# Kernel tuning notes

Measured on AMD Instinct MI355X. Metric: run time of the kernel, lower is better.

The kernel has to match this reference:

```python
import jax, jax.numpy as jnp
import numpy as np

B, S, D, E, H, K = 4, 4096, 256, 8, 512, 2  # batch, seq, d_model, n_experts, ffn_hidden(=2*D), top_k


def setup_inputs() -> dict:
    key = jax.random.key(0)
    ks = jax.random.split(key, 6)
    x = jax.random.normal(ks[0], (B, S, D), jnp.float32)
    Wg = jax.random.normal(ks[1], (D, E), jnp.float32) * 0.02
    bg = jnp.zeros((E,), jnp.float32)
    W1 = jax.random.normal(ks[2], (E, D, H), jnp.float32) * 0.02
    b1 = jnp.zeros((E, H), jnp.float32)
    W2 = jax.random.normal(ks[3], (E, H, D), jnp.float32) * 0.02
    b2 = jnp.zeros((E, D), jnp.float32)
    return {"x": x, "Wg": Wg, "bg": bg, "W1": W1, "b1": b1, "W2": W2, "b2": b2}


def reference(x, Wg, bg, W1, b1, W2, b2):
    Bv, Sv, Dv = x.shape
    # Gate: linear -> top_k indices. NOTE: the original computes softmax(top_k scores)
    # but never uses the probabilities in the combine, so only indices matter.
    gate_scores = x @ Wg + bg                      # [B,S,E]
    _, idx = jax.lax.top_k(gate_scores, K)          # [B,S,K] (distinct experts per token)
    # Boolean membership mask per expert (0/1), matching (expert_indices == i).any(-1)
    mask = jax.nn.one_hot(idx, E, dtype=x.dtype).sum(axis=-2)  # [B,S,E]

    xf = x.reshape(-1, Dv)                          # [T,D]
    mf = mask.reshape(-1, E)                        # [T,E]
    # Dense all-experts FFN, masked combine (faithful to unweighted scatter-add).
    h = jax.nn.gelu(jnp.einsum('td,edh->teh', xf, W1) + b1[None], approximate=False)  # [T,E,H]
    y = jnp.einsum('teh,ehd->ted', h, W2) + b2[None]                                   # [T,E,D]
    out = jnp.einsum('ted,te->td', y, mf)                                              # [T,D]
    return out.reshape(Bv, Sv, Dv)
```

## Files before the change

### kernel.cpp

```cpp
#include <hip/hip_runtime.h>
#include <hip/hip_bf16.h>

#define T_TOK 16384
#define DM 256
#define NE 8
#define HF 512
#define TM 64
#define XS_LD 264
#define HC_LD 264

typedef __bf16 bf16x8 __attribute__((ext_vector_type(8)));
typedef float f32x4 __attribute__((ext_vector_type(4)));
typedef unsigned short u16x8 __attribute__((ext_vector_type(8)));

__device__ __forceinline__ unsigned short f2bf(float f) {
  unsigned u = __float_as_uint(f);
  u += 0x7fffu + ((u >> 16) & 1u);
  return (unsigned short)(u >> 16);
}

__device__ __forceinline__ float gelu_f(float v) {
  float s = fabsf(v) * 0.70710678118654752f;
  float t = __builtin_amdgcn_rcpf(1.0f + 0.3275911f * s);
  float p = t * (0.254829592f +
            t * (-0.284496736f +
            t * (1.421413741f +
            t * (-1.453152027f + t * 1.061405429f))));
  float e = 1.0f - p * __expf(-s * s);
  e = copysignf(e, v);
  return 0.5f * v * (1.0f + e);
}

__global__ __launch_bounds__(256) void gate_kernel(
    const float* __restrict__ x, const float* __restrict__ Wg,
    const float* __restrict__ bg, int* __restrict__ cnts, int* __restrict__ list) {
  __shared__ float wg_s[DM * NE];
  __shared__ int hist[NE], base_s[NE], rank[NE];
  int tid = threadIdx.x;
#pragma unroll
  for (int i = 0; i < NE; i++) wg_s[tid * NE + i] = Wg[tid * NE + i];
  if (tid < NE) { hist[tid] = 0; rank[tid] = 0; }
  __syncthreads();

  int tl = tid >> 2;
  int cg = tid & 3;
  int t = blockIdx.x * 64 + tl;
  const float* xr = x + (size_t)t * DM + cg * 64;
  double acc[NE];
#pragma unroll
  for (int i = 0; i < NE; i++) acc[i] = 0.0;
  for (int d = 0; d < 64; d += 4) {
    float4 xv = *reinterpret_cast<const float4*>(xr + d);
    const float* w0 = &wg_s[(cg * 64 + d) * NE];
#pragma unroll
    for (int i = 0; i < NE; i++) {
      acc[i] += (double)xv.x * (double)w0[i] + (double)xv.y * (double)w0[NE + i] +
                (double)xv.z * (double)w0[2 * NE + i] + (double)xv.w * (double)w0[3 * NE + i];
    }
  }
#pragma unroll
  for (int i = 0; i < NE; i++) {
    acc[i] += __shfl_xor(acc[i], 1, 64);
    acc[i] += __shfl_xor(acc[i], 2, 64);
    acc[i] += (double)bg[i];
  }
  int e1 = 0;
#pragma unroll
  for (int i = 1; i < NE; i++) if (acc[i] > acc[e1]) e1 = i;
  int e2 = -1;
#pragma unroll
  for (int i = 0; i < NE; i++) {
    if (i == e1) continue;
    if (e2 < 0 || acc[i] > acc[e2]) e2 = i;
  }

  if (cg == 0) {
    atomicAdd(&hist[e1], 1);
    atomicAdd(&hist[e2], 1);
  }
  __syncthreads();
  if (tid < NE) base_s[tid] = atomicAdd(&cnts[tid], hist[tid]);
  __syncthreads();
  if (cg == 0) {
    int r1 = atomicAdd(&rank[e1], 1);
    list[e1 * T_TOK + base_s[e1] + r1] = t;
    int r2 = atomicAdd(&rank[e2], 1);
    list[e2 * T_TOK + base_s[e2] + r2] = t;
  }
}

__global__ __launch_bounds__(256) void pack_kernel(
    const float* __restrict__ in, unsigned short* __restrict__ out, int K, int N) {
  int idx = blockIdx.x * 256 + threadIdx.x;
  int n = idx & (N - 1);
  int rest = idx / N;
  int kq = rest & ((K >> 3) - 1);
  int eidx = rest / (K >> 3);
  int k0 = kq * 8;
  const float* src = in + ((size_t)eidx * K + k0) * N + n;
  u16x8 pk;
#pragma unroll
  for (int j = 0; j < 8; j++) pk[j] = f2bf(src[(size_t)j * N]);
  size_t baseo = (size_t)eidx * K * N +
                 (size_t)((n >> 4) * (K >> 5) + (k0 >> 5)) * 512 +
                 (size_t)(((k0 >> 3) & 3) * 128 + (n & 15) * 8);
  *reinterpret_cast<u16x8*>(out + baseo) = pk;
}

__global__ __launch_bounds__(512, 4) void ffn_kernel(
    const float* __restrict__ x, const unsigned short* __restrict__ w1p,
    const float* __restrict__ b1, const unsigned short* __restrict__ w2p,
    const float* __restrict__ b2, const int* __restrict__ cnts,
    const int* __restrict__ list, float* __restrict__ out) {
  __shared__ unsigned short Xs[TM * XS_LD];
  __shared__ unsigned short Hc[TM * HC_LD];
  __shared__ int tok[TM];

  int e = blockIdx.x >> 8;
  int tile = blockIdx.x & 255;
  int cnt = cnts[e];
  int base = tile * TM;
  if (base >= cnt) return;
  int rowsv = min(TM, cnt - base);

  int tid = threadIdx.x;
  {
    int r = tid >> 3, cg = tid & 7;
    int token = -1;
    if (r < rowsv) token = list[e * T_TOK + base + r];
    if (cg == 0) tok[r] = token;
    unsigned short* xrow = &Xs[r * XS_LD + cg * 32];
    if (token >= 0) {
      const float* xr = x + (size_t)token * DM + cg * 32;
#pragma unroll
      for (int j = 0; j < 8; j++) {
        float4 v = *reinterpret_cast<const float4*>(xr + j * 4);
        unsigned long long pk = (unsigned long long)f2bf(v.x) |
                                ((unsigned long long)f2bf(v.y) << 16) |
                                ((unsigned long long)f2bf(v.z) << 32) |
                                ((unsigned long long)f2bf(v.w) << 48);
        *reinterpret_cast<unsigned long long*>(xrow + j * 4) = pk;
      }
    } else {
#pragma unroll
      for (int j = 0; j < 8; j++)
        *reinterpret_cast<unsigned long long*>(xrow + j * 4) = 0ull;
    }
  }
  __syncthreads();

  int w = tid >> 6, lane = tid & 63;
  int quad = lane >> 4, l16 = lane & 15;

  const unsigned short* w1e = w1p + (size_t)e * (HF * DM) + lane * 8;
  const unsigned short* w2e = w2p + (size_t)e * (DM * HF) + lane * 8;

  f32x4 zero4 = {0.f, 0.f, 0.f, 0.f};
  f32x4 oacc[4][2];
#pragma unroll
  for (int mt = 0; mt < 4; mt++)
#pragma unroll
    for (int nt = 0; nt < 2; nt++) oacc[mt][nt] = zero4;

  f32x4 pacc[4][2];

#pragma unroll
  for (int mt = 0; mt < 4; mt++)
#pragma unroll
    for (int nt = 0; nt < 2; nt++) pacc[mt][nt] = zero4;
#pragma unroll
  for (int ks = 0; ks < 8; ks++) {
    bf16x8 a[4], bfr[2];
#pragma unroll
    for (int mt = 0; mt < 4; mt++)
      a[mt] = *reinterpret_cast<const bf16x8*>(&Xs[(mt * 16 + l16) * XS_LD + ks * 32 + quad * 8]);
#pragma unroll
    for (int nt = 0; nt < 2; nt++)
      bfr[nt] = *reinterpret_cast<const bf16x8*>(w1e + (size_t)(((w * 2 + nt) * 8 + ks)) * 512);
#pragma unroll
    for (int nt = 0; nt < 2; nt++)
#pragma unroll
      for (int mt = 0; mt < 4; mt++)
        pacc[mt][nt] = __builtin_amdgcn_mfma_f32_16x16x32_bf16(a[mt], bfr[nt], pacc[mt][nt], 0, 0, 0);
  }
#pragma unroll
  for (int nt = 0; nt < 2; nt++) {
    float bias1 = b1[e * HF + w * 32 + nt * 16 + l16];
#pragma unroll
    for (int mt = 0; mt < 4; mt++)
#pragma unroll
      for (int r = 0; r < 4; r++) {
        int row = mt * 16 + quad * 4 + r;
        Hc[row * HC_LD + w * 32 + nt * 16 + l16] = f2bf(gelu_f(pacc[mt][nt][r] + bias1));
      }
  }
  __syncthreads();

#pragma unroll
  for (int ks2 = 0; ks2 < 8; ks2++) {
    bf16x8 a[4], bfr[2];
#pragma unroll
    for (int mt = 0; mt < 4; mt++)
      a[mt] = *reinterpret_cast<const bf16x8*>(&Hc[(mt * 16 + l16) * HC_LD + ks2 * 32 + quad * 8]);
#pragma unroll
    for (int nt = 0; nt < 2; nt++)
      bfr[nt] = *reinterpret_cast<const bf16x8*>(w2e + (size_t)((w * 2 + nt) * 16 + ks2) * 512);
#pragma unroll
    for (int nt = 0; nt < 2; nt++)
#pragma unroll
      for (int mt = 0; mt < 4; mt++)
        oacc[mt][nt] = __builtin_amdgcn_mfma_f32_16x16x32_bf16(a[mt], bfr[nt], oacc[mt][nt], 0, 0, 0);
  }

#pragma unroll
  for (int mt = 0; mt < 4; mt++)
#pragma unroll
    for (int nt = 0; nt < 2; nt++) pacc[mt][nt] = zero4;
#pragma unroll
  for (int ks = 0; ks < 8; ks++) {
    bf16x8 a[4], bfr[2];
#pragma unroll
    for (int mt = 0; mt < 4; mt++)
      a[mt] = *reinterpret_cast<const bf16x8*>(&Xs[(mt * 16 + l16) * XS_LD + ks * 32 + quad * 8]);
#pragma unroll
    for (int nt = 0; nt < 2; nt++)
      bfr[nt] = *reinterpret_cast<const bf16x8*>(w1e + (size_t)((16 + w * 2 + nt) * 8 + ks) * 512);
#pragma unroll
    for (int nt = 0; nt < 2; nt++)
#pragma unroll
      for (int mt = 0; mt < 4; mt++)
        pacc[mt][nt] = __builtin_amdgcn_mfma_f32_16x16x32_bf16(a[mt], bfr[nt], pacc[mt][nt], 0, 0, 0);
  }
  __syncthreads();

#pragma unroll
  for (int nt = 0; nt < 2; nt++) {
    float bias1 = b1[e * HF + 256 + w * 32 + nt * 16 + l16];
#pragma unroll
    for (int mt = 0; mt < 4; mt++)
#pragma unroll
      for (int r = 0; r < 4; r++) {
        int row = mt * 16 + quad * 4 + r;
        Hc[row * HC_LD + w * 32 + nt * 16 + l16] = f2bf(gelu_f(pacc[mt][nt][r] + bias1));
      }
  }
  __syncthreads();

#pragma unroll
  for (int ks2 = 0; ks2 < 8; ks2++) {
    bf16x8 a[4], bfr[2];
#pragma unroll
    for (int mt = 0; mt < 4; mt++)
      a[mt] = *reinterpret_cast<const bf16x8*>(&Hc[(mt * 16 + l16) * HC_LD + ks2 * 32 + quad * 8]);
#pragma unroll
    for (int nt = 0; nt < 2; nt++)
      bfr[nt] = *reinterpret_cast<const bf16x8*>(w2e + (size_t)((w * 2 + nt) * 16 + 8 + ks2) * 512);
#pragma unroll
    for (int nt = 0; nt < 2; nt++)
#pragma unroll
      for (int mt = 0; mt < 4; mt++)
        oacc[mt][nt] = __builtin_amdgcn_mfma_f32_16x16x32_bf16(a[mt], bfr[nt], oacc[mt][nt], 0, 0, 0);
  }

  float b2v[2];
#pragma unroll
  for (int nt = 0; nt < 2; nt++) b2v[nt] = b2[e * DM + w * 32 + nt * 16 + l16];
#pragma unroll
  for (int mt = 0; mt < 4; mt++) {
#pragma unroll
    for (int r = 0; r < 4; r++) {
      int m = mt * 16 + quad * 4 + r;
      int token = tok[m];
      if (token < 0) continue;
      float* orow = out + (size_t)token * DM;
#pragma unroll
      for (int nt = 0; nt < 2; nt++) {
        int d = w * 32 + nt * 16 + l16;
        atomicAdd(&orow[d], oacc[mt][nt][r] + b2v[nt]);
      }
    }
  }
}

extern "C" void kernel_launch(void* const* d_in, const int* in_sizes, int n_in,
                              void* d_out, int out_size, void* d_ws, size_t ws_size,
                              hipStream_t stream) {
  (void)in_sizes; (void)n_in; (void)ws_size;
  const float* x  = (const float*)d_in[0];
  const float* Wg = (const float*)d_in[1];
  const float* bg = (const float*)d_in[2];
  const float* W1 = (const float*)d_in[3];
  const float* b1 = (const float*)d_in[4];
  const float* W2 = (const float*)d_in[5];
  const float* b2 = (const float*)d_in[6];
  float* out = (float*)d_out;

  char* ws = (char*)d_ws;
  int* cnts = (int*)ws;
  int* list = (int*)(ws + 256);
  unsigned short* w1p = (unsigned short*)(ws + 256 + 524288);
  unsigned short* w2p = (unsigned short*)(ws + 256 + 524288 + 2097152);

  hipMemsetAsync(cnts, 0, 256, stream);
  hipMemsetAsync(d_out, 0, (size_t)out_size * sizeof(float), stream);

  hipLaunchKernelGGL(pack_kernel, dim3(NE * DM * HF / 8 / 256), dim3(256), 0, stream,
                     W1, w1p, DM, HF);
  hipLaunchKernelGGL(pack_kernel, dim3(NE * DM * HF / 8 / 256), dim3(256), 0, stream,
                     W2, w2p, HF, DM);
  hipLaunchKernelGGL(gate_kernel, dim3(T_TOK / 64), dim3(256), 0, stream,
                     x, Wg, bg, cnts, list);
  hipLaunchKernelGGL(ffn_kernel, dim3(NE * 256), dim3(512), 0, stream,
                     x, w1p, b1, w2p, b2, cnts, list, out);
}
```

Measured before the change: 160.6 us.

## Merge prep kernels and software-pipeline weight loads in the expert FFN

After: 152.8 us. -4.8%, faster.

```diff
diff --git a/kernel.cpp b/kernel.cpp
--- a/kernel.cpp
+++ b/kernel.cpp
@@ -7,11 +7,12 @@
 #define HF 512
 #define TM 64
 #define XS_LD 264
-#define HC_LD 264
 
 typedef __bf16 bf16x8 __attribute__((ext_vector_type(8)));
 typedef float f32x4 __attribute__((ext_vector_type(4)));
 typedef unsigned short u16x8 __attribute__((ext_vector_type(8)));
+
+#define MFMA16(a, b, c) __builtin_amdgcn_mfma_f32_16x16x32_bf16((a), (b), (c), 0, 0, 0)
 
 __device__ __forceinline__ unsigned short f2bf(float f) {
   unsigned u = __float_as_uint(f);
@@ -31,67 +32,9 @@
   return 0.5f * v * (1.0f + e);
 }
 
-__global__ __launch_bounds__(256) void gate_kernel(
-    const float* __restrict__ x, const float* __restrict__ Wg,
-    const float* __restrict__ bg, int* __restrict__ cnts, int* __restrict__ list) {
-  __shared__ float wg_s[DM * NE];
-  __shared__ int hist[NE], base_s[NE], rank[NE];
-  int tid = threadIdx.x;
-#pragma unroll
-  for (int i = 0; i < NE; i++) wg_s[tid * NE + i] = Wg[tid * NE + i];
-  if (tid < NE) { hist[tid] = 0; rank[tid] = 0; }
-  __syncthreads();
-
-  int tl = tid >> 2;
-  int cg = tid & 3;
-  int t = blockIdx.x * 64 + tl;
-  const float* xr = x + (size_t)t * DM + cg * 64;
-  double acc[NE];
-#pragma unroll
-  for (int i = 0; i < NE; i++) acc[i] = 0.0;
-  for (int d = 0; d < 64; d += 4) {
-    float4 xv = *reinterpret_cast<const float4*>(xr + d);
-    const float* w0 = &wg_s[(cg * 64 + d) * NE];
-#pragma unroll
-    for (int i = 0; i < NE; i++) {
-      acc[i] += (double)xv.x * (double)w0[i] + (double)xv.y * (double)w0[NE + i] +
-                (double)xv.z * (double)w0[2 * NE + i] + (double)xv.w * (double)w0[3 * NE + i];
-    }
-  }
-#pragma unroll
-  for (int i = 0; i < NE; i++) {
-    acc[i] += __shfl_xor(acc[i], 1, 64);
-    acc[i] += __shfl_xor(acc[i], 2, 64);
-    acc[i] += (double)bg[i];
-  }
-  int e1 = 0;
-#pragma unroll
-  for (int i = 1; i < NE; i++) if (acc[i] > acc[e1]) e1 = i;
-  int e2 = -1;
-#pragma unroll
-  for (int i = 0; i < NE; i++) {
-    if (i == e1) continue;
-    if (e2 < 0 || acc[i] > acc[e2]) e2 = i;
-  }
-
-  if (cg == 0) {
-    atomicAdd(&hist[e1], 1);
-    atomicAdd(&hist[e2], 1);
-  }
-  __syncthreads();
-  if (tid < NE) base_s[tid] = atomicAdd(&cnts[tid], hist[tid]);
-  __syncthreads();
-  if (cg == 0) {
-    int r1 = atomicAdd(&rank[e1], 1);
-    list[e1 * T_TOK + base_s[e1] + r1] = t;
-    int r2 = atomicAdd(&rank[e2], 1);
-    list[e2 * T_TOK + base_s[e2] + r2] = t;
-  }
-}
-
-__global__ __launch_bounds__(256) void pack_kernel(
-    const float* __restrict__ in, unsigned short* __restrict__ out, int K, int N) {
-  int idx = blockIdx.x * 256 + threadIdx.x;
+__device__ __forceinline__ void pack_body(const float* __restrict__ in,
+                                          unsigned short* __restrict__ out,
+                                          int K, int N, int idx) {
   int n = idx & (N - 1);
   int rest = idx / N;
   int kq = rest & ((K >> 3) - 1);
@@ -107,13 +50,82 @@
   *reinterpret_cast<u16x8*>(out + baseo) = pk;
 }
 
+__global__ __launch_bounds__(256) void prep_kernel(
+    const float* __restrict__ W1, const float* __restrict__ W2,
+    unsigned short* __restrict__ w1p, unsigned short* __restrict__ w2p,
+    const float* __restrict__ x, const float* __restrict__ Wg,
+    const float* __restrict__ bg, int* __restrict__ cnts, int* __restrict__ list) {
+  __shared__ float wg_s[DM * NE];
+  __shared__ int hist[NE], base_s[NE], rank[NE];
+  int b = blockIdx.x;
+  int tid = threadIdx.x;
+  if (b < 512) {
+    pack_body(W1, w1p, DM, HF, b * 256 + tid);
+    return;
+  }
+  if (b < 1024) {
+    pack_body(W2, w2p, HF, DM, (b - 512) * 256 + tid);
+    return;
+  }
+  int gb = b - 1024;
+#pragma unroll
+  for (int i = 0; i < NE; i++) wg_s[tid * NE + i] = Wg[tid * NE + i];
+  if (tid < NE) { hist[tid] = 0; rank[tid] = 0; }
+  __syncthreads();
+
+  int tl = tid >> 2;
+  int cg = tid & 3;
+  int t = gb * 64 + tl;
+  const float* xr = x + (size_t)t * DM + cg * 64;
+  double acc[NE];
+#pragma unroll
+  for (int i = 0; i < NE; i++) acc[i] = 0.0;
+  for (int d = 0; d < 64; d += 4) {
+    float4 xv = *reinterpret_cast<const float4*>(xr + d);
+    const float* w0 = &wg_s[(cg * 64 + d) * NE];
+#pragma unroll
+    for (int i = 0; i < NE; i++) {
+      acc[i] += (double)xv.x * (double)w0[i] + (double)xv.y * (double)w0[NE + i] +
+                (double)xv.z * (double)w0[2 * NE + i] + (double)xv.w * (double)w0[3 * NE + i];
+    }
+  }
+#pragma unroll
+  for (int i = 0; i < NE; i++) {
+    acc[i] += __shfl_xor(acc[i], 1, 64);
+    acc[i] += __shfl_xor(acc[i], 2, 64);
+    acc[i] += (double)bg[i];
+  }
+  int e1 = 0;
+#pragma unroll
+  for (int i = 1; i < NE; i++) if (acc[i] > acc[e1]) e1 = i;
+  int e2 = -1;
+#pragma unroll
+  for (int i = 0; i < NE; i++) {
+    if (i == e1) continue;
+    if (e2 < 0 || acc[i] > acc[e2]) e2 = i;
+  }
+  if (cg == 0) {
+    atomicAdd(&hist[e1], 1);
+    atomicAdd(&hist[e2], 1);
+  }
+  __syncthreads();
+  if (tid < NE) base_s[tid] = atomicAdd(&cnts[tid], hist[tid]);
+  __syncthreads();
+  if (cg == 0) {
+    int r1 = atomicAdd(&rank[e1], 1);
+    list[e1 * T_TOK + base_s[e1] + r1] = t;
+    int r2 = atomicAdd(&rank[e2], 1);
+    list[e2 * T_TOK + base_s[e2] + r2] = t;
+  }
+}
+
 __global__ __launch_bounds__(512, 4) void ffn_kernel(
     const float* __restrict__ x, const unsigned short* __restrict__ w1p,
     const float* __restrict__ b1, const unsigned short* __restrict__ w2p,
     const float* __restrict__ b2, const int* __restrict__ cnts,
     const int* __restrict__ list, float* __restrict__ out) {
   __shared__ unsigned short Xs[TM * XS_LD];
-  __shared__ unsigned short Hc[TM * HC_LD];
+  __shared__ unsigned short Hl[TM * XS_LD];
   __shared__ int tok[TM];
 
   int e = blockIdx.x >> 8;
@@ -124,6 +136,15 @@
   int rowsv = min(TM, cnt - base);
 
   int tid = threadIdx.x;
+  int w = tid >> 6, lane = tid & 63;
+  int quad = lane >> 4, l16 = lane & 15;
+
+  const unsigned short* w1e = w1p + (size_t)e * (HF * DM) + lane * 8;
+  const unsigned short* w2e = w2p + (size_t)e * (DM * HF) + lane * 8;
+
+  bf16x8 bcur0 = *reinterpret_cast<const bf16x8*>(w1e + (size_t)((w * 2 + 0) * 8) * 512);
+  bf16x8 bcur1 = *reinterpret_cast<const bf16x8*>(w1e + (size_t)((w * 2 + 1) * 8) * 512);
+
   {
     int r = tid >> 3, cg = tid & 7;
     int token = -1;
@@ -149,39 +170,33 @@
   }
   __syncthreads();
 
-  int w = tid >> 6, lane = tid & 63;
-  int quad = lane >> 4, l16 = lane & 15;
-
-  const unsigned short* w1e = w1p + (size_t)e * (HF * DM) + lane * 8;
-  const unsigned short* w2e = w2p + (size_t)e * (DM * HF) + lane * 8;
-
   f32x4 zero4 = {0.f, 0.f, 0.f, 0.f};
-  f32x4 oacc[4][2];
+  f32x4 pacc[4][2];
+
 #pragma unroll
   for (int mt = 0; mt < 4; mt++)
 #pragma unroll
-    for (int nt = 0; nt < 2; nt++) oacc[mt][nt] = zero4;
-
-  f32x4 pacc[4][2];
-
-#pragma unroll
-  for (int mt = 0; mt < 4; mt++)
-#pragma unroll
     for (int nt = 0; nt < 2; nt++) pacc[mt][nt] = zero4;
 #pragma unroll
   for (int ks = 0; ks < 8; ks++) {
-    bf16x8 a[4], bfr[2];
+    bf16x8 bn0, bn1;
+    if (ks < 7) {
+      bn0 = *reinterpret_cast<const bf16x8*>(w1e + (size_t)((w * 2 + 0) * 8 + ks + 1) * 512);
+      bn1 = *reinterpret_cast<const bf16x8*>(w1e + (size_t)((w * 2 + 1) * 8 + ks + 1) * 512);
+    } else {
+      bn0 = *reinterpret_cast<const bf16x8*>(w1e + (size_t)((16 + w * 2 + 0) * 8) * 512);
+      bn1 = *reinterpret_cast<const bf16x8*>(w1e + (size_t)((16 + w * 2 + 1) * 8) * 512);
+    }
+    bf16x8 a[4];
 #pragma unroll
     for (int mt = 0; mt < 4; mt++)
       a[mt] = *reinterpret_cast<const bf16x8*>(&Xs[(mt * 16 + l16) * XS_LD + ks * 32 + quad * 8]);
 #pragma unroll
-    for (int nt = 0; nt < 2; nt++)
-      bfr[nt] = *reinterpret_cast<const bf16x8*>(w1e + (size_t)(((w * 2 + nt) * 8 + ks)) * 512);
-#pragma unroll
-    for (int nt = 0; nt < 2; nt++)
-#pragma unroll
-      for (int mt = 0; mt < 4; mt++)
-        pacc[mt][nt] = __builtin_amdgcn_mfma_f32_16x16x32_bf16(a[mt], bfr[nt], pacc[mt][nt], 0, 0, 0);
+    for (int mt = 0; mt < 4; mt++) {
+      pacc[mt][0] = MFMA16(a[mt], bcur0, pacc[mt][0]);
+      pacc[mt][1] = MFMA16(a[mt], bcur1, pacc[mt][1]);
+    }
+    bcur0 = bn0; bcur1 = bn1;
   }
 #pragma unroll
   for (int nt = 0; nt < 2; nt++) {
@@ -191,26 +206,9 @@
 #pragma unroll
       for (int r = 0; r < 4; r++) {
         int row = mt * 16 + quad * 4 + r;
-        Hc[row * HC_LD + w * 32 + nt * 16 + l16] = f2bf(gelu_f(pacc[mt][nt][r] + bias1));
+        Hl[row * XS_LD + w * 32 + nt * 16 + l16] = f2bf(gelu_f(pacc[mt][nt][r] + bias1));
       }
   }
-  __syncthreads();
-
-#pragma unroll
-  for (int ks2 = 0; ks2 < 8; ks2++) {
-    bf16x8 a[4], bfr[2];
-#pragma unroll
-    for (int mt = 0; mt < 4; mt++)
-      a[mt] = *reinterpret_cast<const bf16x8*>(&Hc[(mt * 16 + l16) * HC_LD + ks2 * 32 + quad * 8]);
-#pragma unroll
-    for (int nt = 0; nt < 2; nt++)
-      bfr[nt] = *reinterpret_cast<const bf16x8*>(w2e + (size_t)((w * 2 + nt) * 16 + ks2) * 512);
-#pragma unroll
-    for (int nt = 0; nt < 2; nt++)
-#pragma unroll
-      for (int mt = 0; mt < 4; mt++)
-        oacc[mt][nt] = __builtin_amdgcn_mfma_f32_16x16x32_bf16(a[mt], bfr[nt], oacc[mt][nt], 0, 0, 0);
-  }
 
 #pragma unroll
   for (int mt = 0; mt < 4; mt++)
@@ -218,21 +216,26 @@
     for (int nt = 0; nt < 2; nt++) pacc[mt][nt] = zero4;
 #pragma unroll
   for (int ks = 0; ks < 8; ks++) {
-    bf16x8 a[4], bfr[2];
+    bf16x8 bn0, bn1;
+    if (ks < 7) {
+      bn0 = *reinterpret_cast<const bf16x8*>(w1e + (size_t)((16 + w * 2 + 0) * 8 + ks + 1) * 512);
+      bn1 = *reinterpret_cast<const bf16x8*>(w1e + (size_t)((16 + w * 2 + 1) * 8 + ks + 1) * 512);
+    } else {
+      bn0 = *reinterpret_cast<const bf16x8*>(w2e + (size_t)((w * 2 + 0) * 16) * 512);
+      bn1 = *reinterpret_cast<const bf16x8*>(w2e + (size_t)((w * 2 + 1) * 16) * 512);
+    }
+    bf16x8 a[4];
 #pragma unroll
     for (int mt = 0; mt < 4; mt++)
       a[mt] = *reinterpret_cast<const bf16x8*>(&Xs[(mt * 16 + l16) * XS_LD + ks * 32 + quad * 8]);
 #pragma unroll
-    for (int nt = 0; nt < 2; nt++)
-      bfr[nt] = *reinterpret_cast<const bf16x8*>(w1e + (size_t)((16 + w * 2 + nt) * 8 + ks) * 512);
-#pragma unroll
-    for (int nt = 0; nt < 2; nt++)
-#pragma unroll
-      for (int mt = 0; mt < 4; mt++)
-        pacc[mt][nt] = __builtin_amdgcn_mfma_f32_16x16x32_bf16(a[mt], bfr[nt], pacc[mt][nt], 0, 0, 0);
-  }
-  __syncthreads();
-
+    for (int mt = 0; mt < 4; mt++) {
+      pacc[mt][0] = MFMA16(a[mt], bcur0, pacc[mt][0]);
+      pacc[mt][1] = MFMA16(a[mt], bcur1, pacc[mt][1]);
+    }
+    bcur0 = bn0; bcur1 = bn1;
+  }
+  __syncthreads();
 #pragma unroll
   for (int nt = 0; nt < 2; nt++) {
     float bias1 = b1[e * HF + 256 + w * 32 + nt * 16 + l16];
@@ -241,25 +244,35 @@
 #pragma unroll
       for (int r = 0; r < 4; r++) {
         int row = mt * 16 + quad * 4 + r;
-        Hc[row * HC_LD + w * 32 + nt * 16 + l16] = f2bf(gelu_f(pacc[mt][nt][r] + bias1));
+        Xs[row * XS_LD + w * 32 + nt * 16 + l16] = f2bf(gelu_f(pacc[mt][nt][r] + bias1));
       }
   }
   __syncthreads();
 
-#pragma unroll
-  for (int ks2 = 0; ks2 < 8; ks2++) {
-    bf16x8 a[4], bfr[2];
-#pragma unroll
-    for (int mt = 0; mt < 4; mt++)
-      a[mt] = *reinterpret_cast<const bf16x8*>(&Hc[(mt * 16 + l16) * HC_LD + ks2 * 32 + quad * 8]);
-#pragma unroll
-    for (int nt = 0; nt < 2; nt++)
-      bfr[nt] = *reinterpret_cast<const bf16x8*>(w2e + (size_t)((w * 2 + nt) * 16 + 8 + ks2) * 512);
-#pragma unroll
-    for (int nt = 0; nt < 2; nt++)
-#pragma unroll
-      for (int mt = 0; mt < 4; mt++)
-        oacc[mt][nt] = __builtin_amdgcn_mfma_f32_16x16x32_bf16(a[mt], bfr[nt], oacc[mt][nt], 0, 0, 0);
+  f32x4 oacc[4][2];
+#pragma unroll
+  for (int mt = 0; mt < 4; mt++)
+#pragma unroll
+    for (int nt = 0; nt < 2; nt++) oacc[mt][nt] = zero4;
+#pragma unroll
+  for (int ks2 = 0; ks2 < 16; ks2++) {
+    bf16x8 bn0, bn1;
+    if (ks2 < 15) {
+      bn0 = *reinterpret_cast<const bf16x8*>(w2e + (size_t)((w * 2 + 0) * 16 + ks2 + 1) * 512);
+      bn1 = *reinterpret_cast<const bf16x8*>(w2e + (size_t)((w * 2 + 1) * 16 + ks2 + 1) * 512);
+    }
+    const unsigned short* hbase = (ks2 < 8) ? Hl : Xs;
+    int col = (ks2 & 7) * 32 + quad * 8;
+    bf16x8 a[4];
+#pragma unroll
+    for (int mt = 0; mt < 4; mt++)
+      a[mt] = *reinterpret_cast<const bf16x8*>(&hbase[(mt * 16 + l16) * XS_LD + col]);
+#pragma unroll
+    for (int mt = 0; mt < 4; mt++) {
+      oacc[mt][0] = MFMA16(a[mt], bcur0, oacc[mt][0]);
+      oacc[mt][1] = MFMA16(a[mt], bcur1, oacc[mt][1]);
+    }
+    if (ks2 < 15) { bcur0 = bn0; bcur1 = bn1; }
   }
 
   float b2v[2];
@@ -304,12 +317,8 @@
   hipMemsetAsync(cnts, 0, 256, stream);
   hipMemsetAsync(d_out, 0, (size_t)out_size * sizeof(float), stream);
 
-  hipLaunchKernelGGL(pack_kernel, dim3(NE * DM * HF / 8 / 256), dim3(256), 0, stream,
-                     W1, w1p, DM, HF);
-  hipLaunchKernelGGL(pack_kernel, dim3(NE * DM * HF / 8 / 256), dim3(256), 0, stream,
-                     W2, w2p, HF, DM);
-  hipLaunchKernelGGL(gate_kernel, dim3(T_TOK / 64), dim3(256), 0, stream,
-                     x, Wg, bg, cnts, list);
+  hipLaunchKernelGGL(prep_kernel, dim3(1280), dim3(256), 0, stream,
+                     W1, W2, w1p, w2p, x, Wg, bg, cnts, list);
   hipLaunchKernelGGL(ffn_kernel, dim3(NE * 256), dim3(512), 0, stream,
                      x, w1p, b1, w2p, b2, cnts, list, out);
 }
```
